# Optimization experiments

Measured on AMD Instinct MI355X. Metric: run time of the kernel, lower is better.

## Reference

```python
import jax, jax.numpy as jnp
import numpy as np

WINDOW_SIZE = 11
SIGMA = 1.5
DATA_RANGE = 1.0
WEIGHTS = np.array([0.0448, 0.2856, 0.3001, 0.2363, 0.1333], dtype=np.float32)


def _gaussian_window(window_size, sigma, channels, dtype):
    coords = jnp.arange(window_size, dtype=jnp.float32) - window_size // 2
    g = jnp.exp(-(coords ** 2) / (2.0 * sigma ** 2))
    g = g / g.sum()
    w2d = jnp.outer(g, g)  # (K, K)
    # depthwise kernel, OIHW with I=1, O=channels
    return jnp.broadcast_to(w2d, (channels, 1, window_size, window_size)).astype(dtype)


def _dwconv(x, w, channels, pad):
    return jax.lax.conv_general_dilated(
        x, w, window_strides=(1, 1), padding=[(pad, pad), (pad, pad)],
        dimension_numbers=("NCHW", "OIHW", "NCHW"), feature_group_count=channels)


def _avg_pool2(x):
    b, c, h, w = x.shape
    return x.reshape(b, c, h // 2, 2, w // 2, 2).mean(axis=(3, 5))


def setup_inputs() -> dict:
    key = jax.random.key(0)
    k1, k2 = jax.random.split(key)
    shape = (16, 3, 512, 512)
    pred = jax.random.uniform(k1, shape, dtype=jnp.float32)
    target = jax.random.uniform(k2, shape, dtype=jnp.float32)
    return {"pred": pred, "target": target}


def reference(pred, target):
    weights = jnp.asarray(WEIGHTS, dtype=pred.dtype)
    levels = weights.shape[0]
    channels = pred.shape[1]
    pad = WINDOW_SIZE // 2
    window = _gaussian_window(WINDOW_SIZE, SIGMA, channels, pred.dtype)
    C1 = (0.01 * DATA_RANGE) ** 2
    C2 = (0.03 * DATA_RANGE) ** 2

    mcs_vals = []
    msssim_last = None
    for i in range(levels):
        mu_p = _dwconv(pred, window, channels, pad)
        mu_t = _dwconv(target, window, channels, pad)
        mu_pp = mu_p ** 2
        mu_tt = mu_t ** 2
        mu_pt = mu_p * mu_t
        sig_pp = _dwconv(pred ** 2, window, channels, pad) - mu_pp
        sig_tt = _dwconv(target ** 2, window, channels, pad) - mu_tt
        sig_pt = _dwconv(pred * target, window, channels, pad) - mu_pt
        luminance = (2.0 * mu_pt + C1) / (mu_pp + mu_tt + C1)
        cs = (2.0 * sig_pt + C2) / (sig_pp + sig_tt + C2)
        if i == levels - 1:
            msssim_last = (luminance * cs).mean()
        else:
            mcs_vals.append(cs.mean())
        pred = _avg_pool2(pred)
        target = _avg_pool2(target)

    msssim = msssim_last
    for i, mcs in enumerate(mcs_vals):
        msssim = msssim * mcs ** weights[i]
    return 1.0 - msssim
```

## Files before the change

### kernel.cpp

```cpp
#include <hip/hip_runtime.h>
#include <math.h>


#define NIMG 48
#define TWO_C1 2.0e-4f
#define TWO_C2 1.8e-3f

struct CInfo { int base[5]; int cnt[5]; };

#define FOR11(X) X(0) X(1) X(2) X(3) X(4) X(5) X(6) X(7) X(8) X(9) X(10)

#define TAPLOAD_I(K) \
  const float p##K = rpl_[K]; const float t##K = rtl_[K];
#define TAPLOAD_M(K) \
  float p##K, t##K; { \
    const int x_ = gx + (K) - 5; \
    const int xc_ = min(max(x_, 0), W - 1); \
    const float pv_ = rp_[xc_], tv_ = rt_[xc_]; \
    const bool ok_ = ((unsigned)x_ < (unsigned)W); \
    p##K = ok_ ? pv_ : 0.f; t##K = ok_ ? tv_ : 0.f; }

#define HACC(K) { \
    hA_ = __builtin_fmaf(G##K, p##K, hA_); \
    hB_ = __builtin_fmaf(G##K, t##K, hB_); \
    const float u_ = __builtin_fmaf(t##K, t##K, p##K * p##K); \
    hP_ = __builtin_fmaf(G##K, u_, hP_); \
    const float x_ = p##K * t##K; \
    hQ_ = __builtin_fmaf(G##K, x_, hQ_); }

#define DECLR(K) float rA##K = 0.f, rB##K = 0.f, rP##K = 0.f, rQ##K = 0.f;

#define MS_STEP_N(R, SW) do { \
    const int r_ = (R); \
    float hA_ = 0.f, hB_ = 0.f, hP_ = 0.f, hQ_ = 0.f; \
    float pc_ = 0.f, tc_ = 0.f; \
    if ((unsigned)r_ < (unsigned)H) { \
      const float* rp_ = Pi + (size_t)r_ * W; \
      const float* rt_ = Ti + (size_t)r_ * W; \
      if (MASKED) { \
        FOR11(TAPLOAD_M) \
        FOR11(HACC) \
        pc_ = p5; tc_ = t5; \
      } else { \
        const float* rpl_ = rp_ + gx - 5; \
        const float* rtl_ = rt_ + gx - 5; \
        FOR11(TAPLOAD_I) \
        FOR11(HACC) \
        pc_ = p5; tc_ = t5; \
      } \
    } \
    rA##SW = hA_; rB##SW = hB_; rP##SW = hP_; rQ##SW = hQ_; \
    if (DS) { \
      if (r_ >= y0 && r_ < y0 + nout) { \
        if ((r_ & 1) == 0) { pr = pc_; tr = tc_; } \
        else { \
          float sp_ = pr + pc_, st_ = tr + tc_; \
          sp_ += __shfl_xor(sp_, 1, 64); \
          st_ += __shfl_xor(st_, 1, 64); \
          if (((lane & 1) == 0) && (gx < W)) { \
            const size_t o_ = obase + (size_t)(r_ >> 1) * (size_t)(W >> 1) + \
                              (size_t)(gx >> 1); \
            dsP[o_] = sp_ * 0.25f; \
            dsT[o_] = st_ * 0.25f; \
          } } } } \
  } while (0)

#define VSTEP(GK, S) \
    A_ = __builtin_fmaf(GK, rA##S, A_); B_ = __builtin_fmaf(GK, rB##S, B_); \
    P_ = __builtin_fmaf(GK, rP##S, P_); Q_ = __builtin_fmaf(GK, rQ##S, Q_);

#define ROW_N(IROW, SW, S0,S1,S2,S3,S4,S5,S6,S7,S8,S9,S10) do { \
    const int i_ = (IROW); \
    const bool live_ = (i_ < nout); \
    MS_STEP_N(y0 + 5 + i_, SW); \
    float A_ = G0 * rA##S0, B_ = G0 * rB##S0; \
    float P_ = G0 * rP##S0, Q_ = G0 * rQ##S0; \
    VSTEP(G1, S1) VSTEP(G2, S2) VSTEP(G3, S3) VSTEP(G4, S4) VSTEP(G5, S5) \
    VSTEP(G6, S6) VSTEP(G7, S7) VSTEP(G8, S8) VSTEP(G9, S9) VSTEP(G10, S10) \
    const float m_ = A_ * B_; \
    const float q_ = __builtin_fmaf(A_, A_, B_ * B_); \
    const float cn_ = __builtin_fmaf(4.f, Q_ - m_, TWO_C2); \
    const float cd_ = __builtin_fmaf(2.f, P_ - q_, TWO_C2); \
    float val_; \
    if (LAST) { \
      const float ln_ = __builtin_fmaf(4.f, m_, TWO_C1); \
      const float ld_ = __builtin_fmaf(2.f, q_, TWO_C1); \
      val_ = (ln_ * cn_) / (ld_ * cd_); \
    } else { \
      val_ = cn_ / cd_; \
    } \
    if ((!MASKED || gx < W) && live_) sum += val_; \
  } while (0)

template <int MASKED, int DS, int LAST>
__device__ __forceinline__ float strip_run(
    const float* __restrict__ Pi, const float* __restrict__ Ti,
    const int H, const int W, const int y0, const int nout, const int c0,
    float* __restrict__ dsP, float* __restrict__ dsT, const size_t obase,
    const float G0, const float G1, const float G2, const float G3,
    const float G4, const float G5, const float G6, const float G7,
    const float G8, const float G9, const float G10) {
  const int lane = threadIdx.x & 63;
  const int gx = c0 + lane;
  FOR11(DECLR)
  float pr = 0.f, tr = 0.f, sum = 0.f;

  MS_STEP_N(y0 - 5, 0); MS_STEP_N(y0 - 4, 1); MS_STEP_N(y0 - 3, 2);
  MS_STEP_N(y0 - 2, 3); MS_STEP_N(y0 - 1, 4); MS_STEP_N(y0 + 0, 5);
  MS_STEP_N(y0 + 1, 6); MS_STEP_N(y0 + 2, 7); MS_STEP_N(y0 + 3, 8);
  MS_STEP_N(y0 + 4, 9);

  for (int base = 0; base < nout; base += 11) {
    ROW_N(base + 0, 10, 0,1,2,3,4,5,6,7,8,9,10);
    ROW_N(base + 1, 0,  1,2,3,4,5,6,7,8,9,10,0);
    ROW_N(base + 2, 1,  2,3,4,5,6,7,8,9,10,0,1);
    ROW_N(base + 3, 2,  3,4,5,6,7,8,9,10,0,1,2);
    ROW_N(base + 4, 3,  4,5,6,7,8,9,10,0,1,2,3);
    ROW_N(base + 5, 4,  5,6,7,8,9,10,0,1,2,3,4);
    ROW_N(base + 6, 5,  6,7,8,9,10,0,1,2,3,4,5);
    ROW_N(base + 7, 6,  7,8,9,10,0,1,2,3,4,5,6);
    ROW_N(base + 8, 7,  8,9,10,0,1,2,3,4,5,6,7);
    ROW_N(base + 9, 8,  9,10,0,1,2,3,4,5,6,7,8);
    ROW_N(base + 10, 9, 10,0,1,2,3,4,5,6,7,8,9);
  }
  return sum;
}

template <int DS, int LAST>
__global__ __launch_bounds__(256)
void msssim_level_k(const float* __restrict__ P, const float* __restrict__ T,
                    const int H, const int W, const int strips,
                    const int chunks, const int chunkH, const int tasks,
                    float* __restrict__ dsP, float* __restrict__ dsT,
                    double* __restrict__ partial,
                    const float G0, const float G1, const float G2,
                    const float G3, const float G4, const float G5,
                    const float G6, const float G7, const float G8,
                    const float G9, const float G10) {
  __shared__ float sRed[4];
  const int tid = threadIdx.x;
  const int lane = tid & 63;
  const int wid = tid >> 6;
  float sum = 0.f;
  const int task = blockIdx.x * 4 + wid;
  if (task < tasks) {
    const int strip = task % strips;
    const int rem = task / strips;
    const int chunk = rem % chunks;
    const int img = rem / chunks;
    const int y0 = chunk * chunkH;
    const int nout = min(chunkH, H - y0);
    const size_t ibase = (size_t)img * H * W;
    const size_t obase = DS ? (size_t)img * (size_t)(H >> 1) * (W >> 1) : 0;
    const bool edge = (strip == 0) || (strip * 64 + 69 > W);
    if (edge)
      sum = strip_run<1, DS, LAST>(P + ibase, T + ibase, H, W, y0, nout,
                                   strip * 64, dsP, dsT, obase,
                                   G0, G1, G2, G3, G4, G5, G6, G7, G8, G9, G10);
    else
      sum = strip_run<0, DS, LAST>(P + ibase, T + ibase, H, W, y0, nout,
                                   strip * 64, dsP, dsT, obase,
                                   G0, G1, G2, G3, G4, G5, G6, G7, G8, G9, G10);
  }
#pragma unroll
  for (int off = 32; off; off >>= 1) sum += __shfl_down(sum, off, 64);
  if (lane == 0) sRed[wid] = sum;
  __syncthreads();
  if (tid == 0)
    partial[blockIdx.x] = (double)(sRed[0] + sRed[1] + sRed[2] + sRed[3]);
}

__global__ void msssim_combine_k(const double* __restrict__ partial,
                                 float* __restrict__ out, const CInfo ci) {
  const int lane = threadIdx.x & 63;
  double lv[5];
#pragma unroll
  for (int L = 0; L < 5; ++L) {
    double s = 0.0;
    for (int i = lane; i < ci.cnt[L]; i += 64) s += partial[ci.base[L] + i];
#pragma unroll
    for (int off = 32; off; off >>= 1) s += __shfl_down(s, off, 64);
    lv[L] = s;
  }
  if (lane == 0) {
    double ms = lv[4] / (48.0 * 32.0 * 32.0);
    ms *= pow(lv[0] / (48.0 * 512.0 * 512.0), (double)0.0448f);
    ms *= pow(lv[1] / (48.0 * 256.0 * 256.0), (double)0.2856f);
    ms *= pow(lv[2] / (48.0 * 128.0 * 128.0), (double)0.3001f);
    ms *= pow(lv[3] / (48.0 * 64.0 * 64.0),  (double)0.2363f);
    out[0] = (float)(1.0 - ms);
  }
}

extern "C" void kernel_launch(void* const* d_in, const int* in_sizes, int n_in,
                              void* d_out, int out_size, void* d_ws, size_t ws_size,
                              hipStream_t stream) {
  const float* pred = (const float*)d_in[0];
  const float* targ = (const float*)d_in[1];
  float* out = (float*)d_out;

  char* ws = (char*)d_ws;
  double* partial = (double*)ws;
  size_t off = 32768;
  auto alloc = [&](size_t elems) {
    float* p = (float*)(ws + off);
    off += elems * sizeof(float);
    return p;
  };
  float* L1p = alloc((size_t)NIMG * 256 * 256);
  float* L1t = alloc((size_t)NIMG * 256 * 256);
  float* L2p = alloc((size_t)NIMG * 128 * 128);
  float* L2t = alloc((size_t)NIMG * 128 * 128);
  float* L3p = alloc((size_t)NIMG * 64 * 64);
  float* L3t = alloc((size_t)NIMG * 64 * 64);
  float* L4p = alloc((size_t)NIMG * 32 * 32);
  float* L4t = alloc((size_t)NIMG * 32 * 32);

  float g[11];
  {
    double gd[11], s = 0.0;
    for (int k = 0; k < 11; ++k) {
      const double c = (double)(k - 5);
      gd[k] = exp(-(c * c) / 4.5);
      s += gd[k];
    }
    for (int k = 0; k < 11; ++k) g[k] = (float)(gd[k] / s);
  }

  CInfo ci;
  int slotOff = 0;

  auto launchLevel = [&](const float* P, const float* T, int H, int W,
                         int chunkH, float* dP, float* dT, int L, bool last) {
    const int strips = (W + 63) / 64;
    const int chunks = (H + chunkH - 1) / chunkH;
    const int tasks = strips * chunks * NIMG;
    const int blocks = (tasks + 3) / 4;
    ci.base[L] = slotOff;
    ci.cnt[L] = blocks;
    if (last) {
      msssim_level_k<0, 1><<<blocks, 256, 0, stream>>>(
          P, T, H, W, strips, chunks, chunkH, tasks, nullptr, nullptr,
          partial + slotOff, g[0], g[1], g[2], g[3], g[4], g[5], g[6], g[7],
          g[8], g[9], g[10]);
    } else {
      msssim_level_k<1, 0><<<blocks, 256, 0, stream>>>(
          P, T, H, W, strips, chunks, chunkH, tasks, dP, dT,
          partial + slotOff, g[0], g[1], g[2], g[3], g[4], g[5], g[6], g[7],
          g[8], g[9], g[10]);
    }
    slotOff += blocks;
  };

  launchLevel(pred, targ, 512, 512, 32, L1p, L1t, 0, false);
  launchLevel(L1p, L1t, 256, 256, 16, L2p, L2t, 1, false);
  launchLevel(L2p, L2t, 128, 128, 8, L3p, L3t, 2, false);
  launchLevel(L3p, L3t, 64, 64, 8, L4p, L4t, 3, false);
  launchLevel(L4p, L4t, 32, 32, 8, nullptr, nullptr, 4, true);

  msssim_combine_k<<<1, 64, 0, stream>>>(partial, out, ci);
}
```

Baseline: 184.5 us.

## Compute two adjacent output columns per thread for the full-resolution level

Adds a new level kernel in which each lane handles two neighbouring output columns. It loads 12 taps per row instead of 11 per column, shares those loads and the squared/cross products between both columns, and writes the 2x2 downsample directly. Only the 512x512 level uses it. This roughly halves redundant global loads and product computations per output. The cost is doubled register state (eight ring buffers of 11 values each), which may reduce occupancy or cause spills, and fewer tasks per level.

```diff
diff --git a/kernel.cpp b/kernel.cpp
--- a/kernel.cpp
+++ b/kernel.cpp
@@ -9,6 +9,7 @@
 struct CInfo { int base[5]; int cnt[5]; };
 
 #define FOR11(X) X(0) X(1) X(2) X(3) X(4) X(5) X(6) X(7) X(8) X(9) X(10)
+#define FOR12(X) FOR11(X) X(11)
 
 #define TAPLOAD_I(K) \
   const float p##K = rpl_[K]; const float t##K = rtl_[K];
@@ -170,6 +171,191 @@
     partial[blockIdx.x] = (double)(sRed[0] + sRed[1] + sRed[2] + sRed[3]);
 }
 
+#define T2I(K) \
+  const float p##K = rpl_[K]; const float t##K = rtl_[K];
+#define T2M(K) \
+  float p##K, t##K; { \
+    const int x_ = x0 + (K) - 5; \
+    const int xc_ = min(max(x_, 0), W - 1); \
+    const float pv_ = rp_[xc_], tv_ = rt_[xc_]; \
+    const bool ok_ = ((unsigned)x_ < (unsigned)W); \
+    p##K = ok_ ? pv_ : 0.f; t##K = ok_ ? tv_ : 0.f; }
+#define FLD2(K) \
+  const float u##K = __builtin_fmaf(t##K, t##K, p##K * p##K); \
+  const float xx##K = p##K * t##K;
+#define H2A(GK, K) \
+  hA_ = __builtin_fmaf(GK, p##K, hA_); hB_ = __builtin_fmaf(GK, t##K, hB_); \
+  hP_ = __builtin_fmaf(GK, u##K, hP_); hQ_ = __builtin_fmaf(GK, xx##K, hQ_);
+#define H2B(GK, K) \
+  jA_ = __builtin_fmaf(GK, p##K, jA_); jB_ = __builtin_fmaf(GK, t##K, jB_); \
+  jP_ = __builtin_fmaf(GK, u##K, jP_); jQ_ = __builtin_fmaf(GK, xx##K, jQ_);
+#define H2ALL \
+  H2A(G0,0) H2A(G1,1) H2A(G2,2) H2A(G3,3) H2A(G4,4) H2A(G5,5) \
+  H2A(G6,6) H2A(G7,7) H2A(G8,8) H2A(G9,9) H2A(G10,10) \
+  H2B(G0,1) H2B(G1,2) H2B(G2,3) H2B(G3,4) H2B(G4,5) H2B(G5,6) \
+  H2B(G6,7) H2B(G7,8) H2B(G8,9) H2B(G9,10) H2B(G10,11)
+
+#define DECLR2(K) \
+  float rA##K = 0.f, rB##K = 0.f, rP##K = 0.f, rQ##K = 0.f; \
+  float yA##K = 0.f, yB##K = 0.f, yP##K = 0.f, yQ##K = 0.f;
+
+#define MS2_STEP(R, SW) do { \
+    const int r_ = (R); \
+    float hA_ = 0.f, hB_ = 0.f, hP_ = 0.f, hQ_ = 0.f; \
+    float jA_ = 0.f, jB_ = 0.f, jP_ = 0.f, jQ_ = 0.f; \
+    float pc0_ = 0.f, tc0_ = 0.f, pc1_ = 0.f, tc1_ = 0.f; \
+    if ((unsigned)r_ < (unsigned)H) { \
+      const float* rp_ = Pi + (size_t)r_ * W; \
+      const float* rt_ = Ti + (size_t)r_ * W; \
+      if (MASKED) { \
+        FOR12(T2M) \
+        FOR12(FLD2) \
+        H2ALL \
+        pc0_ = p5; tc0_ = t5; pc1_ = p6; tc1_ = t6; \
+      } else { \
+        const float* rpl_ = rp_ + x0 - 5; \
+        const float* rtl_ = rt_ + x0 - 5; \
+        FOR12(T2I) \
+        FOR12(FLD2) \
+        H2ALL \
+        pc0_ = p5; tc0_ = t5; pc1_ = p6; tc1_ = t6; \
+      } \
+    } \
+    rA##SW = hA_; rB##SW = hB_; rP##SW = hP_; rQ##SW = hQ_; \
+    yA##SW = jA_; yB##SW = jB_; yP##SW = jP_; yQ##SW = jQ_; \
+    if (DS) { \
+      if (r_ >= y0 && r_ < y0 + nout) { \
+        if ((r_ & 1) == 0) { pr0 = pc0_; tr0 = tc0_; pr1 = pc1_; tr1 = tc1_; } \
+        else if (x0 < W) { \
+          const float sp_ = (pr0 + pc0_) + (pr1 + pc1_); \
+          const float st_ = (tr0 + tc0_) + (tr1 + tc1_); \
+          const size_t o_ = obase + (size_t)(r_ >> 1) * (size_t)(W >> 1) + \
+                            (size_t)(x0 >> 1); \
+          dsP[o_] = sp_ * 0.25f; \
+          dsT[o_] = st_ * 0.25f; \
+        } } } \
+  } while (0)
+
+#define V2STEP(GK, S) \
+    A_ = __builtin_fmaf(GK, rA##S, A_); B_ = __builtin_fmaf(GK, rB##S, B_); \
+    P_ = __builtin_fmaf(GK, rP##S, P_); Q_ = __builtin_fmaf(GK, rQ##S, Q_); \
+    C_ = __builtin_fmaf(GK, yA##S, C_); D_ = __builtin_fmaf(GK, yB##S, D_); \
+    E_ = __builtin_fmaf(GK, yP##S, E_); F_ = __builtin_fmaf(GK, yQ##S, F_);
+
+#define ROW2_N(IROW, SW, S0,S1,S2,S3,S4,S5,S6,S7,S8,S9,S10) do { \
+    const int i_ = (IROW); \
+    const bool live_ = (i_ < nout); \
+    MS2_STEP(y0 + 5 + i_, SW); \
+    float A_ = G0 * rA##S0, B_ = G0 * rB##S0; \
+    float P_ = G0 * rP##S0, Q_ = G0 * rQ##S0; \
+    float C_ = G0 * yA##S0, D_ = G0 * yB##S0; \
+    float E_ = G0 * yP##S0, F_ = G0 * yQ##S0; \
+    V2STEP(G1, S1) V2STEP(G2, S2) V2STEP(G3, S3) V2STEP(G4, S4) \
+    V2STEP(G5, S5) V2STEP(G6, S6) V2STEP(G7, S7) V2STEP(G8, S8) \
+    V2STEP(G9, S9) V2STEP(G10, S10) \
+    const float mA_ = A_ * B_; \
+    const float qA_ = __builtin_fmaf(A_, A_, B_ * B_); \
+    const float cnA_ = __builtin_fmaf(4.f, Q_ - mA_, TWO_C2); \
+    const float cdA_ = __builtin_fmaf(2.f, P_ - qA_, TWO_C2); \
+    const float mB_ = C_ * D_; \
+    const float qB_ = __builtin_fmaf(C_, C_, D_ * D_); \
+    const float cnB_ = __builtin_fmaf(4.f, F_ - mB_, TWO_C2); \
+    const float cdB_ = __builtin_fmaf(2.f, E_ - qB_, TWO_C2); \
+    float vA_, vB_; \
+    if (LAST) { \
+      vA_ = (__builtin_fmaf(4.f, mA_, TWO_C1) * cnA_) / \
+            (__builtin_fmaf(2.f, qA_, TWO_C1) * cdA_); \
+      vB_ = (__builtin_fmaf(4.f, mB_, TWO_C1) * cnB_) / \
+            (__builtin_fmaf(2.f, qB_, TWO_C1) * cdB_); \
+    } else { \
+      vA_ = cnA_ / cdA_; \
+      vB_ = cnB_ / cdB_; \
+    } \
+    if (live_) { \
+      if (!MASKED || x0 < W) sum += vA_; \
+      if (!MASKED || x0 + 1 < W) sum += vB_; \
+    } \
+  } while (0)
+
+template <int MASKED, int DS, int LAST>
+__device__ __forceinline__ float strip_run2(
+    const float* __restrict__ Pi, const float* __restrict__ Ti,
+    const int H, const int W, const int y0, const int nout, const int c0,
+    float* __restrict__ dsP, float* __restrict__ dsT, const size_t obase,
+    const float G0, const float G1, const float G2, const float G3,
+    const float G4, const float G5, const float G6, const float G7,
+    const float G8, const float G9, const float G10) {
+  const int lane = threadIdx.x & 63;
+  const int x0 = c0 + 2 * lane;
+  FOR11(DECLR2)
+  float pr0 = 0.f, tr0 = 0.f, pr1 = 0.f, tr1 = 0.f, sum = 0.f;
+
+  MS2_STEP(y0 - 5, 0); MS2_STEP(y0 - 4, 1); MS2_STEP(y0 - 3, 2);
+  MS2_STEP(y0 - 2, 3); MS2_STEP(y0 - 1, 4); MS2_STEP(y0 + 0, 5);
+  MS2_STEP(y0 + 1, 6); MS2_STEP(y0 + 2, 7); MS2_STEP(y0 + 3, 8);
+  MS2_STEP(y0 + 4, 9);
+
+  for (int base = 0; base < nout; base += 11) {
+    ROW2_N(base + 0, 10, 0,1,2,3,4,5,6,7,8,9,10);
+    ROW2_N(base + 1, 0,  1,2,3,4,5,6,7,8,9,10,0);
+    ROW2_N(base + 2, 1,  2,3,4,5,6,7,8,9,10,0,1);
+    ROW2_N(base + 3, 2,  3,4,5,6,7,8,9,10,0,1,2);
+    ROW2_N(base + 4, 3,  4,5,6,7,8,9,10,0,1,2,3);
+    ROW2_N(base + 5, 4,  5,6,7,8,9,10,0,1,2,3,4);
+    ROW2_N(base + 6, 5,  6,7,8,9,10,0,1,2,3,4,5);
+    ROW2_N(base + 7, 6,  7,8,9,10,0,1,2,3,4,5,6);
+    ROW2_N(base + 8, 7,  8,9,10,0,1,2,3,4,5,6,7);
+    ROW2_N(base + 9, 8,  9,10,0,1,2,3,4,5,6,7,8);
+    ROW2_N(base + 10, 9, 10,0,1,2,3,4,5,6,7,8,9);
+  }
+  return sum;
+}
+
+template <int DS, int LAST>
+__global__ __launch_bounds__(256)
+void msssim_level2_k(const float* __restrict__ P, const float* __restrict__ T,
+                     const int H, const int W, const int strips,
+                     const int chunks, const int chunkH, const int tasks,
+                     float* __restrict__ dsP, float* __restrict__ dsT,
+                     double* __restrict__ partial,
+                     const float G0, const float G1, const float G2,
+                     const float G3, const float G4, const float G5,
+                     const float G6, const float G7, const float G8,
+                     const float G9, const float G10) {
+  __shared__ float sRed[4];
+  const int tid = threadIdx.x;
+  const int lane = tid & 63;
+  const int wid = tid >> 6;
+  float sum = 0.f;
+  const int task = blockIdx.x * 4 + wid;
+  if (task < tasks) {
+    const int strip = task % strips;
+    const int rem = task / strips;
+    const int chunk = rem % chunks;
+    const int img = rem / chunks;
+    const int y0 = chunk * chunkH;
+    const int nout = min(chunkH, H - y0);
+    const size_t ibase = (size_t)img * H * W;
+    const size_t obase = DS ? (size_t)img * (size_t)(H >> 1) * (W >> 1) : 0;
+    const int sx = strip * 128;
+    const bool edge = (sx < 5) || (sx + 133 > W);
+    if (edge)
+      sum = strip_run2<1, DS, LAST>(P + ibase, T + ibase, H, W, y0, nout, sx,
+                                    dsP, dsT, obase,
+                                    G0, G1, G2, G3, G4, G5, G6, G7, G8, G9, G10);
+    else
+      sum = strip_run2<0, DS, LAST>(P + ibase, T + ibase, H, W, y0, nout, sx,
+                                    dsP, dsT, obase,
+                                    G0, G1, G2, G3, G4, G5, G6, G7, G8, G9, G10);
+  }
+#pragma unroll
+  for (int off = 32; off; off >>= 1) sum += __shfl_down(sum, off, 64);
+  if (lane == 0) sRed[wid] = sum;
+  __syncthreads();
+  if (tid == 0)
+    partial[blockIdx.x] = (double)(sRed[0] + sRed[1] + sRed[2] + sRed[3]);
+}
+
 __global__ void msssim_combine_k(const double* __restrict__ partial,
                                  float* __restrict__ out, const CInfo ci) {
   const int lane = threadIdx.x & 63;
@@ -229,6 +415,20 @@
 
   CInfo ci;
   int slotOff = 0;
+
+  {
+    const int strips = (512 + 127) / 128;
+    const int chunks = 512 / 32;
+    const int tasks = strips * chunks * NIMG;
+    const int blocks = (tasks + 3) / 4;
+    ci.base[0] = slotOff;
+    ci.cnt[0] = blocks;
+    msssim_level2_k<1, 0><<<blocks, 256, 0, stream>>>(
+        pred, targ, 512, 512, strips, chunks, 32, tasks, L1p, L1t,
+        partial + slotOff, g[0], g[1], g[2], g[3], g[4], g[5], g[6], g[7],
+        g[8], g[9], g[10]);
+    slotOff += blocks;
+  }
 
   auto launchLevel = [&](const float* P, const float* T, int H, int W,
                          int chunkH, float* dP, float* dT, int L, bool last) {
@@ -252,7 +452,6 @@
     slotOff += blocks;
   };
 
-  launchLevel(pred, targ, 512, 512, 32, L1p, L1t, 0, false);
   launchLevel(L1p, L1t, 256, 256, 16, L2p, L2t, 1, false);
   launchLevel(L2p, L2t, 128, 128, 8, L3p, L3t, 2, false);
   launchLevel(L3p, L3t, 64, 64, 8, L4p, L4t, 3, false);
```

New measurement: 203.0 us. 1.1x slower.
